# Kernel tuning notes

Measured on AMD Instinct MI355X. Metric: run time of the kernel, lower is better.

The kernel has to match this reference:

```python
import jax, jax.numpy as jnp
import numpy as np

N, E, D, H = 50000, 800000, 64, 4  # nodes, edges, hidden_dim (=edge_hidden_dim=out), heads
NEG_SLOPE = 0.2  # DGL EGATConv leaky_relu default


def setup_inputs() -> dict:
    key = jax.random.key(0)
    ks = jax.random.split(key, 12)
    s = 1.0 / np.sqrt(D)
    sm = 1.0 / np.sqrt(H * D)
    return {
        "h_E": jax.random.normal(ks[0], (N, D), jnp.float32),      # node feats
        "h_H": jax.random.normal(ks[1], (E, D), jnp.float32),      # edge feats
        "src": jax.random.randint(ks[2], (E,), 0, N),
        "dst": jax.random.randint(ks[3], (E,), 0, N),
        "W_node": jax.random.normal(ks[4], (D, H * D), jnp.float32) * s,
        "b_node": jnp.zeros((H * D,), jnp.float32),
        "W_ni": jax.random.normal(ks[5], (D, H * D), jnp.float32) * s,
        "W_nj": jax.random.normal(ks[6], (D, H * D), jnp.float32) * s,
        "W_fij": jax.random.normal(ks[7], (D, H * D), jnp.float32) * s,
        "attn": jax.random.normal(ks[8], (H, D), jnp.float32) * s,
        "Wp_node": jax.random.normal(ks[9], (H * D, D), jnp.float32) * sm,
        "bp_node": jnp.zeros((D,), jnp.float32),
        "Wp_edge": jax.random.normal(ks[10], (H * D, D), jnp.float32) * sm,
        "bp_edge": jnp.zeros((D,), jnp.float32),
    }


def reference(h_E, h_H, src, dst, W_node, b_node, W_ni, W_nj, W_fij, attn,
              Wp_node, bp_node, Wp_edge, bp_edge):
    # EGAT edge update: f_ij = LeakyReLU(fc_ni(h_i) + fc_nj(h_j) + fc_fij(e_ij))
    f = (h_E @ W_ni)[src] + (h_E @ W_nj)[dst] + h_H @ W_fij          # (E, H*D)
    f = jax.nn.leaky_relu(f, NEG_SLOPE).reshape(E, H, D)
    # per-head attention logit and edge-softmax grouped by destination node
    e = jnp.einsum('ehd,hd->eh', f, attn)                            # (E, H)
    emax = jax.ops.segment_max(e, dst, num_segments=N)               # (N, H)
    a = jnp.exp(e - emax[dst])
    a = a / jax.ops.segment_sum(a, dst, num_segments=N)[dst]         # (E, H)
    # attention-weighted aggregation of projected source nodes
    h_proj = (h_E @ W_node + b_node).reshape(N, H, D)
    agg = jax.ops.segment_sum(h_proj[src] * a[:, :, None], dst, num_segments=N)  # (N, H, D)
    # merge heads back to hidden dims, then residual add
    hE_new = agg.reshape(N, H * D) @ Wp_node + bp_node
    hH_new = f.reshape(E, H * D) @ Wp_edge + bp_edge
    return h_E + hE_new, h_H + hH_new
```

## Files before the change

### kernel.cpp

```cpp
#include <hip/hip_runtime.h>
#include <math.h>

#define NEG_SLOPE 0.2f

typedef __bf16 bf16x8 __attribute__((ext_vector_type(8)));
typedef float f32x4 __attribute__((ext_vector_type(4)));
typedef float f32x4v __attribute__((ext_vector_type(4)));

__device__ __forceinline__ ushort f2bf(float x) {
  union { float f; unsigned u; } v; v.f = x;
  unsigned r = v.u + 0x7fffu + ((v.u >> 16) & 1u);
  return (ushort)(r >> 16);
}
__device__ __forceinline__ float bf2f(ushort b) {
  union { unsigned u; float f; } v; v.u = (unsigned)b << 16;
  return v.f;
}

__device__ __forceinline__ int swz(int m) {
  return ((m & 7) << 4) | (((m >> 3) & 3) << 7);
}

__global__ void k_prep(const float* __restrict__ Wfij,
                       const float* __restrict__ Wni,
                       const float* __restrict__ Wnj,
                       const float* __restrict__ Wpe,
                       ushort* __restrict__ WcatT, ushort* __restrict__ WpeT) {
  int i = blockIdx.x * 256 + threadIdx.x;
  if (i < 49152) {
    int c = i / 192, k = i % 192;
    float v = (k < 64) ? Wfij[k * 256 + c]
            : (k < 128) ? Wni[(k - 64) * 256 + c]
                        : Wnj[(k - 128) * 256 + c];
    WcatT[c * 192 + k] = f2bf(v);
  }
  if (i < 16384) {
    int k2 = i >> 6, n2 = i & 63;
    WpeT[n2 * 256 + k2] = f2bf(Wpe[i]);
  }
}

__global__ __launch_bounds__(256) void k_node(
    const float* __restrict__ hE,
    const float* __restrict__ Wnode, const float* __restrict__ bnode,
    const float* __restrict__ Wpn,
    ushort* __restrict__ hE_bf, ushort* __restrict__ hq, int n) {
  __shared__ float hEt[64 * 36];
  __shared__ float hpl[32 * 260];
  const int tid = threadIdx.x;
  const int n0 = blockIdx.x * 32;

#pragma unroll
  for (int i = 0; i < 8; ++i) {
    int flat = tid + i * 256;
    int m = flat >> 6, k = flat & 63;
    float v = (n0 + m < n) ? hE[(size_t)(n0 + m) * 64 + k] : 0.f;
    hEt[k * 36 + m] = v;
    if (n0 + m < n) hE_bf[(size_t)(n0 + m) * 64 + k] = f2bf(v);
  }
  __syncthreads();

  const int tm = tid >> 5, tc = tid & 31, c0 = tc * 8;

  {
    float acc[4][8];
#pragma unroll
    for (int mm = 0; mm < 4; ++mm)
#pragma unroll
      for (int j = 0; j < 8; ++j) acc[mm][j] = 0.f;

    for (int k = 0; k < 64; ++k) {
      float4 h4 = *(const float4*)&hEt[k * 36 + tm * 4];
      float4 w0 = *(const float4*)&Wnode[k * 256 + c0];
      float4 w1 = *(const float4*)&Wnode[k * 256 + c0 + 4];
      float hv[4] = {h4.x, h4.y, h4.z, h4.w};
      float wv[8] = {w0.x, w0.y, w0.z, w0.w, w1.x, w1.y, w1.z, w1.w};
#pragma unroll
      for (int mm = 0; mm < 4; ++mm)
#pragma unroll
        for (int j = 0; j < 8; ++j) acc[mm][j] += hv[mm] * wv[j];
    }
#pragma unroll
    for (int mm = 0; mm < 4; ++mm) {
      int m = tm * 4 + mm;
#pragma unroll
      for (int j = 0; j < 8; ++j)
        hpl[m * 260 + c0 + j] = acc[mm][j] + bnode[c0 + j];
    }
  }
  __syncthreads();

  const int hh = tc >> 3, dc0 = (tc & 7) * 8;
  float acc[4][8];
#pragma unroll
  for (int mm = 0; mm < 4; ++mm)
#pragma unroll
    for (int j = 0; j < 8; ++j) acc[mm][j] = 0.f;

  for (int k = 0; k < 64; ++k) {
    float4 w0 = *(const float4*)&Wpn[(size_t)(hh * 64 + k) * 64 + dc0];
    float4 w1 = *(const float4*)&Wpn[(size_t)(hh * 64 + k) * 64 + dc0 + 4];
    float wv[8] = {w0.x, w0.y, w0.z, w0.w, w1.x, w1.y, w1.z, w1.w};
#pragma unroll
    for (int mm = 0; mm < 4; ++mm) {
      float hv = hpl[(tm * 4 + mm) * 260 + hh * 64 + k];
#pragma unroll
      for (int j = 0; j < 8; ++j) acc[mm][j] += hv * wv[j];
    }
  }
#pragma unroll
  for (int mm = 0; mm < 4; ++mm) {
    int m = tm * 4 + mm;
    if (n0 + m < n) {
      ushort u[8];
#pragma unroll
      for (int j = 0; j < 8; ++j) u[j] = f2bf(acc[mm][j]);
      *(uint4*)&hq[(size_t)(n0 + m) * 256 + c0] = *(const uint4*)u;
    }
  }
}

__global__ void k_zero(int* __restrict__ deg, int n) {
  int g = blockIdx.x * 256 + threadIdx.x;
  if (g < n) deg[g] = 0;
}

__global__ void k_hist(const int* __restrict__ dst, int* __restrict__ deg,
                       int E) {
  int g = blockIdx.x * 256 + threadIdx.x;
  if (g < E) atomicAdd(&deg[dst[g]], 1);
}

__global__ __launch_bounds__(1024) void k_scanA(const int* __restrict__ deg,
                                                int* __restrict__ off,
                                                int* __restrict__ btot, int n) {
  __shared__ int sbuf[1024];
  int t = threadIdx.x, g = blockIdx.x * 1024 + t;
  int v = (g < n) ? deg[g] : 0;
  sbuf[t] = v;
  __syncthreads();
  for (int ofs = 1; ofs < 1024; ofs <<= 1) {
    int x = (t >= ofs) ? sbuf[t - ofs] : 0;
    __syncthreads();
    sbuf[t] += x;
    __syncthreads();
  }
  if (g < n) off[g] = sbuf[t] - v;
  if (t == 1023) btot[blockIdx.x] = sbuf[t];
}

__global__ void k_scanB(const int* __restrict__ btot, int* __restrict__ boff,
                        int nb) {
  if (threadIdx.x == 0 && blockIdx.x == 0) {
    int acc = 0;
    for (int b = 0; b < nb; ++b) { boff[b] = acc; acc += btot[b]; }
  }
}

__global__ void k_scanC(int* __restrict__ off, const int* __restrict__ boff,
                        int* __restrict__ cursor, int n, int E) {
  int g = blockIdx.x * 1024 + threadIdx.x;
  if (g < n) {
    int v = off[g] + boff[g >> 10];
    off[g] = v;
    cursor[g] = v;
  }
  if (g == n) off[n] = E;
}

__global__ void k_scatter(const int* __restrict__ dst,
                          const int* __restrict__ src,
                          int* __restrict__ cursor, int* __restrict__ rank,
                          int* __restrict__ srcs, int E) {
  int g = blockIdx.x * 256 + threadIdx.x;
  if (g < E) {
    int pos = atomicAdd(&cursor[dst[g]], 1);
    rank[g] = pos;
    srcs[pos] = src[g];
  }
}

__global__ __launch_bounds__(256, 2) void k_edge(
    const float* __restrict__ hH,
    const int* __restrict__ src, const int* __restrict__ dst,
    const ushort* __restrict__ WcatT,
    const float* __restrict__ attn,
    const ushort* __restrict__ WpeT,
    const float* __restrict__ bpe,
    const ushort* __restrict__ hE_bf,
    const int* __restrict__ rank,
    float* __restrict__ e_ws,
    float* __restrict__ out1, int ntiles) {
  __shared__ __align__(16) char smem[32 * 384 + 32 * 512 + 128];
  char* ab = smem;
  char* fb = smem + 12288;
  int* rkbuf = (int*)(smem + 28672);

  const int tid = threadIdx.x;
  const int w = tid >> 6, l = tid & 63;
  const int lr = l & 15, lk = l >> 4;
  const int swa = (lr & 7) << 4;
  const int stm = tid >> 3, sts = tid & 7;
  const int swm = (stm & 7) << 4;

  bf16x8 bw1[6][4];
#pragma unroll
  for (int ks = 0; ks < 6; ++ks)
#pragma unroll
    for (int nt = 0; nt < 4; ++nt)
      bw1[ks][nt] = *(const bf16x8*)(WcatT +
          (size_t)(w * 64 + nt * 16 + lr) * 192 + ks * 32 + lk * 8);
  bf16x8 bw2[8];
#pragma unroll
  for (int ks = 0; ks < 8; ++ks)
    bw2[ks] = *(const bf16x8*)(WpeT +
        (size_t)(w * 16 + lr) * 256 + ks * 32 + lk * 8);
  float av[4];
#pragma unroll
  for (int nt = 0; nt < 4; ++nt) av[nt] = attn[w * 64 + nt * 16 + lr];
  const float bpv = bpe[w * 16 + lr];
  const int sw0 = swz(lr), sw1 = swz(16 + lr);

  for (int tile = blockIdx.x; tile < ntiles; tile += gridDim.x) {
    const int e0 = tile * 32;

    if (tid < 32) rkbuf[tid] = rank[e0 + tid];
    {
      int sn = src[e0 + stm], dn = dst[e0 + stm];
      char* arow = ab + stm * 384;
      const f32x4v* p =
          (const f32x4v*)(hH + (size_t)(e0 + stm) * 64 + sts * 8);
      f32x4v x = __builtin_nontemporal_load(p);
      f32x4v y = __builtin_nontemporal_load(p + 1);
      ushort u[8] = {f2bf(x[0]), f2bf(x[1]), f2bf(x[2]), f2bf(x[3]),
                     f2bf(y[0]), f2bf(y[1]), f2bf(y[2]), f2bf(y[3])};
      *(uint4*)(arow + ((sts * 16) ^ swm)) = *(const uint4*)u;
      *(uint4*)(arow + (128 + ((sts * 16) ^ swm))) =
          *(const uint4*)(hE_bf + (size_t)sn * 64 + sts * 8);
      *(uint4*)(arow + (256 + ((sts * 16) ^ swm))) =
          *(const uint4*)(hE_bf + (size_t)dn * 64 + sts * 8);
    }
    __syncthreads();

    f32x4 acc[2][4];
#pragma unroll
    for (int mt = 0; mt < 2; ++mt)
#pragma unroll
      for (int nt = 0; nt < 4; ++nt) acc[mt][nt] = (f32x4){0.f, 0.f, 0.f, 0.f};

#pragma unroll
    for (int ks = 0; ks < 6; ++ks) {
      int sec = (ks >> 1) << 7;
      int off = ((ks & 1) << 6) | (lk << 4);
      bf16x8 a0 = *(const bf16x8*)(ab + lr * 384 + sec + (off ^ swa));
      bf16x8 a1 = *(const bf16x8*)(ab + (16 + lr) * 384 + sec + (off ^ swa));
#pragma unroll
      for (int nt = 0; nt < 4; ++nt) {
        acc[0][nt] = __builtin_amdgcn_mfma_f32_16x16x32_bf16(
            a0, bw1[ks][nt], acc[0][nt], 0, 0, 0);
        acc[1][nt] = __builtin_amdgcn_mfma_f32_16x16x32_bf16(
            a1, bw1[ks][nt], acc[1][nt], 0, 0, 0);
      }
    }

    float pkeep[2][4];
#pragma unroll
    for (int mt = 0; mt < 2; ++mt) {
#pragma unroll
      for (int r = 0; r < 4; ++r) {
        int m = mt * 16 + lk * 4 + r;
        char* rowp = fb + m * 512;
        int sw = swz(m);
        float p = 0.f;
#pragma unroll
        for (int nt = 0; nt < 4; ++nt) {
          int c = w * 64 + nt * 16 + lr;
          float v = acc[mt][nt][r];
          v = (v >= 0.f) ? v : NEG_SLOPE * v;
          p += v * av[nt];
          *(ushort*)(rowp + ((c * 2) ^ sw)) = f2bf(v);
        }
        p += __shfl_xor(p, 1);
        p += __shfl_xor(p, 2);
        p += __shfl_xor(p, 4);
        p += __shfl_xor(p, 8);
        pkeep[mt][r] = p;
      }
    }
    __syncthreads();

    f32x4 acc2[2];
    acc2[0] = (f32x4){0.f, 0.f, 0.f, 0.f};
    acc2[1] = (f32x4){0.f, 0.f, 0.f, 0.f};
#pragma unroll
    for (int ks = 0; ks < 8; ++ks) {
      int ko = (ks * 32 + lk * 8) * 2;
      bf16x8 a0 = *(const bf16x8*)(fb + lr * 512 + (ko ^ sw0));
      bf16x8 a1 = *(const bf16x8*)(fb + (16 + lr) * 512 + (ko ^ sw1));
      acc2[0] =
          __builtin_amdgcn_mfma_f32_16x16x32_bf16(a0, bw2[ks], acc2[0], 0, 0, 0);
      acc2[1] =
          __builtin_amdgcn_mfma_f32_16x16x32_bf16(a1, bw2[ks], acc2[1], 0, 0, 0);
    }

#pragma unroll
    for (int mt = 0; mt < 2; ++mt)
#pragma unroll
      for (int r = 0; r < 4; ++r) {
        int m = mt * 16 + lk * 4 + r;
        int swmr = (m & 7) << 4;
        ushort h =
            *(const ushort*)(ab + m * 384 + ((((w * 16 + lr) * 2)) ^ swmr));
        size_t idx = (size_t)(e0 + m) * 64 + w * 16 + lr;
        __builtin_nontemporal_store(acc2[mt][r] + bf2f(h) + bpv, &out1[idx]);
      }
    if (lr == 0) {
#pragma unroll
      for (int mt = 0; mt < 2; ++mt)
#pragma unroll
        for (int r = 0; r < 4; ++r) {
          int m = mt * 16 + lk * 4 + r;
          e_ws[(size_t)rkbuf[m] * 4 + w] = pkeep[mt][r];
        }
    }
    __syncthreads();
  }
}

__global__ __launch_bounds__(256) void k3_csr(
    const int* __restrict__ csr_off, const float* __restrict__ e_ws,
    const int* __restrict__ srcs, const ushort* __restrict__ hq,
    const float* __restrict__ hE, const float* __restrict__ bpn,
    float* __restrict__ out0, int n) {
  int node = blockIdx.x * 4 + (threadIdx.x >> 6);
  if (node >= n) return;
  int d = threadIdx.x & 63;
  int beg = csr_off[node], end = csr_off[node + 1];
  float base = hE[(size_t)node * 64 + d] + bpn[d];
  if (beg == end) {
    out0[(size_t)node * 64 + d] = base;
    return;
  }
  float s0 = 0.f, s1 = 0.f, s2 = 0.f, s3 = 0.f;
  float y0 = 0.f, y1 = 0.f, y2 = 0.f, y3 = 0.f;
  for (int i = beg; i < end; ++i) {
    f32x4 ev = *(const f32x4*)(e_ws + (size_t)i * 4);
    int sn = srcs[i];
    float w0 = __expf(ev[0] - 12.f);
    float w1 = __expf(ev[1] - 12.f);
    float w2 = __expf(ev[2] - 12.f);
    float w3 = __expf(ev[3] - 12.f);
    s0 += w0; s1 += w1; s2 += w2; s3 += w3;
    const ushort* hp = hq + (size_t)sn * 256;
    y0 += w0 * bf2f(hp[d]);
    y1 += w1 * bf2f(hp[64 + d]);
    y2 += w2 * bf2f(hp[128 + d]);
    y3 += w3 * bf2f(hp[192 + d]);
  }
  float y = y0 / s0 + y1 / s1 + y2 / s2 + y3 / s3;
  out0[(size_t)node * 64 + d] = base + y;
}

extern "C" void kernel_launch(void* const* d_in, const int* in_sizes, int n_in,
                              void* d_out, int out_size, void* d_ws, size_t ws_size,
                              hipStream_t stream) {
  const float* h_E    = (const float*)d_in[0];
  const float* h_H    = (const float*)d_in[1];
  const int*   src    = (const int*)d_in[2];
  const int*   dst    = (const int*)d_in[3];
  const float* W_node = (const float*)d_in[4];
  const float* b_node = (const float*)d_in[5];
  const float* W_ni   = (const float*)d_in[6];
  const float* W_nj   = (const float*)d_in[7];
  const float* W_fij  = (const float*)d_in[8];
  const float* attn   = (const float*)d_in[9];
  const float* Wp_node= (const float*)d_in[10];
  const float* bp_node= (const float*)d_in[11];
  const float* Wp_edge= (const float*)d_in[12];
  const float* bp_edge= (const float*)d_in[13];

  const int n = in_sizes[0] / 64;
  const int e = in_sizes[1] / 64;
  const int nscan = (n + 1023) / 1024;

  ushort* ws_hEbf = (ushort*)d_ws;
  ushort* ws_hq   = ws_hEbf + (size_t)n * 64;
  float*  ws_e    = (float*)(ws_hq + (size_t)n * 256);
  int*    ws_deg  = (int*)(ws_e + (size_t)e * 4);
  int*    ws_off  = ws_deg + n;
  int*    ws_cur  = ws_off + n + 1;
  int*    ws_btot = ws_cur + n;
  int*    ws_boff = ws_btot + 64;
  int*    ws_rank = ws_boff + 64;
  int*    ws_srcs = ws_rank + e;
  ushort* ws_Wcat = (ushort*)(ws_srcs + e);
  ushort* ws_WpeT = ws_Wcat + 49152;

  float* out0 = (float*)d_out;
  float* out1 = out0 + (size_t)n * 64;

  k_prep<<<192, 256, 0, stream>>>(W_fij, W_ni, W_nj, Wp_edge, ws_Wcat, ws_WpeT);
  {
    int blocks = (n + 31) / 32;
    k_node<<<blocks, 256, 0, stream>>>(h_E, W_node, b_node, Wp_node,
                                       ws_hEbf, ws_hq, n);
  }
  k_zero<<<(n + 255) / 256, 256, 0, stream>>>(ws_deg, n);
  k_hist<<<(e + 255) / 256, 256, 0, stream>>>(dst, ws_deg, e);
  k_scanA<<<nscan, 1024, 0, stream>>>(ws_deg, ws_off, ws_btot, n);
  k_scanB<<<1, 64, 0, stream>>>(ws_btot, ws_boff, nscan);
  k_scanC<<<nscan, 1024, 0, stream>>>(ws_off, ws_boff, ws_cur, n, e);
  k_scatter<<<(e + 255) / 256, 256, 0, stream>>>(dst, src, ws_cur, ws_rank,
                                                 ws_srcs, e);
  {
    int ntiles = e / 32;
    k_edge<<<1024, 256, 0, stream>>>(h_H, src, dst, ws_Wcat, attn, ws_WpeT,
                                     bp_edge, ws_hEbf, ws_rank, ws_e, out1,
                                     ntiles);
  }
  {
    int blocks = (n + 3) / 4;
    k3_csr<<<blocks, 256, 0, stream>>>(ws_off, ws_e, ws_srcs, ws_hq, h_E,
                                       bp_node, out0, n);
  }
}
```

Measured before the change: 462.8 us.

## Prefetch next edge tile into registers and fold degree zeroing into prep kernel

The edge kernel now issues the global loads for the next tile (hH rows, gathered bf16 node rows, rank) right after the barrier. They complete while the current tile's MFMA work runs, so load latency is hidden behind compute instead of being exposed at the top of each iteration. This costs about 16 extra live registers per thread, which could reduce occupancy. On the last iteration it reloads the current tile rather than branching. Separately, zeroing of the degree array moves into k_prep with a slightly larger grid, removing one kernel launch. That grid size is hard-coded to cover this node count.

```diff
diff --git a/kernel.cpp b/kernel.cpp
--- a/kernel.cpp
+++ b/kernel.cpp
@@ -25,7 +25,8 @@
                        const float* __restrict__ Wni,
                        const float* __restrict__ Wnj,
                        const float* __restrict__ Wpe,
-                       ushort* __restrict__ WcatT, ushort* __restrict__ WpeT) {
+                       ushort* __restrict__ WcatT, ushort* __restrict__ WpeT,
+                       int* __restrict__ deg, int n) {
   int i = blockIdx.x * 256 + threadIdx.x;
   if (i < 49152) {
     int c = i / 192, k = i % 192;
@@ -38,6 +39,7 @@
     int k2 = i >> 6, n2 = i & 63;
     WpeT[n2 * 256 + k2] = f2bf(Wpe[i]);
   }
+  if (i < n) deg[i] = 0;
 }
 
 __global__ __launch_bounds__(256) void k_node(
@@ -118,11 +120,6 @@
       *(uint4*)&hq[(size_t)(n0 + m) * 256 + c0] = *(const uint4*)u;
     }
   }
-}
-
-__global__ void k_zero(int* __restrict__ deg, int n) {
-  int g = blockIdx.x * 256 + threadIdx.x;
-  if (g < n) deg[g] = 0;
 }
 
 __global__ void k_hist(const int* __restrict__ dst, int* __restrict__ deg,
@@ -221,26 +218,45 @@
   const float bpv = bpe[w * 16 + lr];
   const int sw0 = swz(lr), sw1 = swz(16 + lr);
 
-  for (int tile = blockIdx.x; tile < ntiles; tile += gridDim.x) {
+  f32x4v sx, sy;
+  uint4 si, sj;
+  int srk = 0;
+
+#define ISSUE_STAGE(T)                                                        \
+  {                                                                           \
+    int ee0 = (T) * 32;                                                       \
+    int sn_ = src[ee0 + stm], dn_ = dst[ee0 + stm];                           \
+    const f32x4v* p_ =                                                        \
+        (const f32x4v*)(hH + (size_t)(ee0 + stm) * 64 + sts * 8);             \
+    sx = __builtin_nontemporal_load(p_);                                      \
+    sy = __builtin_nontemporal_load(p_ + 1);                                  \
+    si = *(const uint4*)(hE_bf + (size_t)sn_ * 64 + sts * 8);                 \
+    sj = *(const uint4*)(hE_bf + (size_t)dn_ * 64 + sts * 8);                 \
+    if (tid < 32) srk = rank[ee0 + tid];                                      \
+  }
+
+  int tile = blockIdx.x;
+  if (tile < ntiles) ISSUE_STAGE(tile);
+
+  for (; tile < ntiles; tile += gridDim.x) {
     const int e0 = tile * 32;
 
-    if (tid < 32) rkbuf[tid] = rank[e0 + tid];
     {
-      int sn = src[e0 + stm], dn = dst[e0 + stm];
       char* arow = ab + stm * 384;
-      const f32x4v* p =
-          (const f32x4v*)(hH + (size_t)(e0 + stm) * 64 + sts * 8);
-      f32x4v x = __builtin_nontemporal_load(p);
-      f32x4v y = __builtin_nontemporal_load(p + 1);
-      ushort u[8] = {f2bf(x[0]), f2bf(x[1]), f2bf(x[2]), f2bf(x[3]),
-                     f2bf(y[0]), f2bf(y[1]), f2bf(y[2]), f2bf(y[3])};
+      ushort u[8] = {f2bf(sx[0]), f2bf(sx[1]), f2bf(sx[2]), f2bf(sx[3]),
+                     f2bf(sy[0]), f2bf(sy[1]), f2bf(sy[2]), f2bf(sy[3])};
       *(uint4*)(arow + ((sts * 16) ^ swm)) = *(const uint4*)u;
-      *(uint4*)(arow + (128 + ((sts * 16) ^ swm))) =
-          *(const uint4*)(hE_bf + (size_t)sn * 64 + sts * 8);
-      *(uint4*)(arow + (256 + ((sts * 16) ^ swm))) =
-          *(const uint4*)(hE_bf + (size_t)dn * 64 + sts * 8);
+      *(uint4*)(arow + (128 + ((sts * 16) ^ swm))) = si;
+      *(uint4*)(arow + (256 + ((sts * 16) ^ swm))) = sj;
+      if (tid < 32) rkbuf[tid] = srk;
     }
     __syncthreads();
+
+    {
+      int nxt = tile + gridDim.x;
+      if (nxt >= ntiles) nxt = tile;
+      ISSUE_STAGE(nxt);
+    }
 
     f32x4 acc[2][4];
 #pragma unroll
@@ -325,6 +341,7 @@
     }
     __syncthreads();
   }
+#undef ISSUE_STAGE
 }
 
 __global__ __launch_bounds__(256) void k3_csr(
@@ -399,13 +416,13 @@
   float* out0 = (float*)d_out;
   float* out1 = out0 + (size_t)n * 64;
 
-  k_prep<<<192, 256, 0, stream>>>(W_fij, W_ni, W_nj, Wp_edge, ws_Wcat, ws_WpeT);
+  k_prep<<<196, 256, 0, stream>>>(W_fij, W_ni, W_nj, Wp_edge, ws_Wcat,
+                                  ws_WpeT, ws_deg, n);
   {
     int blocks = (n + 31) / 32;
     k_node<<<blocks, 256, 0, stream>>>(h_E, W_node, b_node, Wp_node,
                                        ws_hEbf, ws_hq, n);
   }
-  k_zero<<<(n + 255) / 256, 256, 0, stream>>>(ws_deg, n);
   k_hist<<<(e + 255) / 256, 256, 0, stream>>>(dst, ws_deg, e);
   k_scanA<<<nscan, 1024, 0, stream>>>(ws_deg, ws_off, ws_btot, n);
   k_scanB<<<1, 64, 0, stream>>>(ws_btot, ws_boff, nscan);
```

New measurement: 566.7 us. 22.5% more time.
